# Optimization experiments

Hardware: AMD Instinct MI355X
Metric: run time of the kernel (lower is better)

The kernel has to match this reference:

```python
import jax, jax.numpy as jnp
import numpy as np

GROUP_SIZE = 128
IN_FEATURES = 4096
OUT_FEATURES = 4096
BATCH, SEQ = 4, 2048


def setup_inputs() -> dict:
    key = jax.random.key(0)
    k1, k2, k3, k4 = jax.random.split(key, 4)
    x = jax.random.normal(k1, (BATCH, SEQ, IN_FEATURES), dtype=jnp.float32)
    # packed int4 pairs: values in [0, 256), semantics of uint8
    weight_packed = jax.random.randint(k2, (OUT_FEATURES, IN_FEATURES // 2), 0, 256, dtype=jnp.int32)
    groups = IN_FEATURES // GROUP_SIZE  # 32
    scales = jax.random.uniform(k3, (OUT_FEATURES, groups), dtype=jnp.float32) * 0.02 + 0.001
    zeros = jnp.zeros((OUT_FEATURES, groups), dtype=jnp.float32)  # unused in forward (as in source)
    bias = jax.random.normal(k4, (OUT_FEATURES,), dtype=jnp.float32)
    return {"x": x, "weight_packed": weight_packed, "scales": scales, "zeros": zeros, "bias": bias}


def _unpack_int4(packed, K):
    # low nibble -> even columns, high nibble -> odd columns; values shifted to [-8, 7]
    low = (packed & 15) - 8
    high = ((packed >> 4) & 15) - 8
    M = packed.shape[0]
    return jnp.stack([low, high], axis=-1).reshape(M, K)  # interleave [l0,h0,l1,h1,...]


def reference(x, weight_packed, scales, zeros, bias):
    K = IN_FEATURES
    groups = K // GROUP_SIZE
    w_int = _unpack_int4(weight_packed, K)  # [O, K] int
    w_grouped = w_int.astype(jnp.float32).reshape(OUT_FEATURES, groups, GROUP_SIZE)
    w = (w_grouped * scales[:, :, None]).reshape(OUT_FEATURES, K).astype(x.dtype)
    # F.linear: x @ w^T + bias
    return jnp.einsum('bsk,ok->bso', x, w) + bias
```

## Files before the change

kernel.cpp:

```cpp
#include <hip/hip_runtime.h>


typedef int i32x4 __attribute__((ext_vector_type(4)));

#define GAS __attribute__((address_space(1)))
#define LAS __attribute__((address_space(3)))

static constexpr int M_DIM = 8192;
static constexpr int N_DIM = 4096;
static constexpr int K_DIM = 4096;

__global__ __launch_bounds__(256) void quant_x(const float* __restrict__ x,
                                               signed char* __restrict__ xq,
                                               float* __restrict__ sx) {
    const int row = blockIdx.x;
    const int tid = threadIdx.x;
    const float* xr = x + (size_t)row * K_DIM;
    float4 v[4];
#pragma unroll
    for (int i = 0; i < 4; ++i) v[i] = *(const float4*)(xr + i * 1024 + tid * 4);
    float m = 0.f;
#pragma unroll
    for (int i = 0; i < 4; ++i)
        m = fmaxf(m, fmaxf(fmaxf(fabsf(v[i].x), fabsf(v[i].y)),
                           fmaxf(fabsf(v[i].z), fabsf(v[i].w))));
#pragma unroll
    for (int off = 32; off >= 1; off >>= 1) m = fmaxf(m, __shfl_xor(m, off, 64));
    __shared__ float wm[4];
    if ((tid & 63) == 0) wm[tid >> 6] = m;
    __syncthreads();
    m = fmaxf(fmaxf(wm[0], wm[1]), fmaxf(wm[2], wm[3]));
    const float inv = 127.f / m;
    if (tid == 0) sx[row] = m / 127.f;
#pragma unroll
    for (int i = 0; i < 4; ++i) {
        int b0 = (int)rintf(v[i].x * inv) & 255;
        int b1 = (int)rintf(v[i].y * inv) & 255;
        int b2 = (int)rintf(v[i].z * inv) & 255;
        int b3 = (int)rintf(v[i].w * inv) & 255;
        *(int*)(xq + (size_t)row * K_DIM + i * 1024 + tid * 4) =
            b0 | (b1 << 8) | (b2 << 16) | (b3 << 24);
    }
}

__global__ __launch_bounds__(256) void unpack_w(const int* __restrict__ wp,
                                                signed char* __restrict__ wq) {
    const int t = blockIdx.x * 256 + threadIdx.x;
    int4 p = *(const int4*)(wp + (size_t)t * 4);
    int pv[4] = {p.x, p.y, p.z, p.w};
    int w01 = (((pv[0] & 15) - 8) & 255) | (((((pv[0] >> 4) & 15) - 8) & 255) << 8) |
              ((((pv[1] & 15) - 8) & 255) << 16) | (((((pv[1] >> 4) & 15) - 8) & 255) << 24);
    int w23 = (((pv[2] & 15) - 8) & 255) | (((((pv[2] >> 4) & 15) - 8) & 255) << 8) |
              ((((pv[3] & 15) - 8) & 255) << 16) | (((((pv[3] >> 4) & 15) - 8) & 255) << 24);
    *(int2*)(wq + (size_t)t * 8) = make_int2(w01, w23);
}

__global__ __launch_bounds__(256) void transp_scales(const float* __restrict__ s,
                                                     float* __restrict__ st) {
    const int t = blockIdx.x * 256 + threadIdx.x;
    st[(size_t)(t & 31) * N_DIM + (t >> 5)] = s[t];
}


#define STAGE_AH(BUF, H, TAU) do { \
  _Pragma("unroll") \
  for (int r_ = 0; r_ < 2; ++r_) { \
    const int g_ = r_ * 8 + wv; \
    const int rbase_ = (g_ >> 2) * 64 + (H) * 32 + (g_ & 3) * 8; \
    const int c_ = (l & 7) ^ (l >> 3); \
    const signed char* sA_ = Aq + (size_t)(m0 + rbase_ + (l >> 3)) * K_DIM \
                                + (size_t)(TAU) * 128 + c_ * 16; \
    __builtin_amdgcn_global_load_lds((const GAS void*)sA_, \
        (LAS void*)(lds + (BUF) * 32768 + rbase_ * 128), 16, 0, 0); \
  } \
} while (0)

#define STAGE_BH(BUF, H, TAU) do { \
    const int rbase_ = (wv >> 2) * 64 + (H) * 32 + (wv & 3) * 8; \
    const int c_ = (l & 7) ^ (l >> 3); \
    const signed char* sB_ = Bq + (size_t)(n0 + rbase_ + (l >> 3)) * K_DIM \
                                + (size_t)(TAU) * 128 + c_ * 16; \
    __builtin_amdgcn_global_load_lds((const GAS void*)sB_, \
        (LAS void*)(lds + 65536 + (BUF) * 16384 + rbase_ * 128), 16, 0, 0); \
} while (0)

#define LOAD_SJ(DST, G) do { \
  _Pragma("unroll") \
  for (int j_ = 0; j_ < 4; ++j_) \
    DST[j_] = scalesT[(size_t)(G) * N_DIM + n0 + wc * 64 + j_ * 16 + lr]; \
} while (0)

#define PHASE(B, MH, NH, S0, S1) do { \
  i32x4 aF0_[2], aF1_[2], bF0_[2], bF1_[2]; \
  _Pragma("unroll") \
  for (int nj = 0; nj < 2; ++nj) { \
    const int rb = wc * 64 + (NH) * 32 + nj * 16 + lr; \
    const signed char* bp = lds + 65536 + (B) * 16384 + rb * 128; \
    bF0_[nj] = *(const i32x4*)(bp + ((quad       ^ (rb & 7)) << 4)); \
    bF1_[nj] = *(const i32x4*)(bp + (((4 | quad) ^ (rb & 7)) << 4)); \
  } \
  _Pragma("unroll") \
  for (int mi = 0; mi < 2; ++mi) { \
    const int ra = wr * 64 + (MH) * 32 + mi * 16 + lr; \
    const signed char* ap = lds + (B) * 32768 + ra * 128; \
    aF0_[mi] = *(const i32x4*)(ap + ((quad       ^ (ra & 7)) << 4)); \
    aF1_[mi] = *(const i32x4*)(ap + (((4 | quad) ^ (ra & 7)) << 4)); \
  } \
  i32x4 ci_[2][2]; \
  __builtin_amdgcn_s_setprio(1); \
  _Pragma("unroll") \
  for (int mi = 0; mi < 2; ++mi) { \
    ci_[mi][0] = __builtin_amdgcn_mfma_i32_16x16x64_i8(aF0_[mi], bF0_[0], izero, 0, 0, 0); \
    ci_[mi][1] = __builtin_amdgcn_mfma_i32_16x16x64_i8(aF0_[mi], bF0_[1], izero, 0, 0, 0); \
  } \
  _Pragma("unroll") \
  for (int mi = 0; mi < 2; ++mi) { \
    ci_[mi][0] = __builtin_amdgcn_mfma_i32_16x16x64_i8(aF1_[mi], bF1_[0], ci_[mi][0], 0, 0, 0); \
    ci_[mi][1] = __builtin_amdgcn_mfma_i32_16x16x64_i8(aF1_[mi], bF1_[1], ci_[mi][1], 0, 0, 0); \
  } \
  __builtin_amdgcn_s_setprio(0); \
  _Pragma("unroll") \
  for (int mi = 0; mi < 2; ++mi) \
    _Pragma("unroll") \
    for (int r = 0; r < 4; ++r) { \
      accf[(MH) * 2 + mi][(NH) * 2 + 0][r] += (S0) * (float)ci_[mi][0][r]; \
      accf[(MH) * 2 + mi][(NH) * 2 + 1][r] += (S1) * (float)ci_[mi][1][r]; \
    } \
} while (0)

#define VMW(N) asm volatile("s_waitcnt vmcnt(" #N ")" ::: "memory")
#define CLB()  asm volatile("" ::: "memory")
#define BAR()  __builtin_amdgcn_s_barrier()

__global__ __launch_bounds__(512)
__attribute__((amdgpu_waves_per_eu(2, 2)))
void gemm_i8(const signed char* __restrict__ Aq,
             const signed char* __restrict__ Bq,
             const float* __restrict__ scalesT,
             const float* __restrict__ sx,
             const float* __restrict__ bias,
             float* __restrict__ C) {
    __shared__ signed char lds[98304];

    const int tid  = threadIdx.x;
    const int l    = tid & 63;
    const int wv   = tid >> 6;
    const int wr   = wv >> 1;
    const int wc   = wv & 1;
    const int lr   = l & 15;
    const int quad = l >> 4;

    const int bid = blockIdx.x;
    const int xcd = bid & 7, kk = bid >> 3;
    const int by = (xcd >> 1) * 8 + (kk & 7);
    const int bx = (xcd & 1) * 16 + (kk >> 3);
    const int m0 = by * 256, n0 = bx * 128;

    float accf[4][4][4];
#pragma unroll
    for (int i = 0; i < 4; ++i)
#pragma unroll
        for (int j = 0; j < 4; ++j)
#pragma unroll
            for (int r = 0; r < 4; ++r) accf[i][j][r] = 0.f;

    const i32x4 izero = {0, 0, 0, 0};
    float sjc0[4], sjc1[4], sjn0[4], sjn1[4];

    LOAD_SJ(sjc0, 0);
    LOAD_SJ(sjc1, 1);
    STAGE_AH(0, 0, 0);
    STAGE_BH(0, 0, 0);
    STAGE_BH(0, 1, 0);
    STAGE_AH(0, 1, 0);
    VMW(3);
    BAR();

#pragma unroll 1
    for (int it = 0; it < 16; ++it) {
        const int tb  = it * 2 + 1;
        const int tn0 = (it * 2 + 2) & 31;
        const int tn1 = (it * 2 + 3) & 31;

        STAGE_AH(1, 0, tb); LOAD_SJ(sjn0, tn0);
        PHASE(0, 0, 0, sjc0[0], sjc0[1]);
        VMW(8); BAR();

        STAGE_BH(1, 0, tb);
        PHASE(0, 0, 1, sjc0[2], sjc0[3]);
        VMW(7); BAR();

        STAGE_BH(1, 1, tb);
        PHASE(0, 1, 0, sjc0[0], sjc0[1]);
        CLB(); BAR();

        STAGE_AH(1, 1, tb);
        PHASE(0, 1, 1, sjc0[2], sjc0[3]);
        VMW(3); BAR();

        STAGE_AH(0, 0, tn0); LOAD_SJ(sjn1, tn1);
        PHASE(1, 0, 0, sjc1[0], sjc1[1]);
        VMW(8); BAR();

        STAGE_BH(0, 0, tn0);
        PHASE(1, 0, 1, sjc1[2], sjc1[3]);
        VMW(7); BAR();

        STAGE_BH(0, 1, tn0);
        PHASE(1, 1, 0, sjc1[0], sjc1[1]);
        CLB(); BAR();

        STAGE_AH(0, 1, tn0);
        PHASE(1, 1, 1, sjc1[2], sjc1[3]);
        VMW(3); BAR();

#pragma unroll
        for (int j = 0; j < 4; ++j) { sjc0[j] = sjn0[j]; sjc1[j] = sjn1[j]; }
    }

    asm volatile("s_waitcnt vmcnt(0)" ::: "memory");

    float sxr[4][4];
#pragma unroll
    for (int i = 0; i < 4; ++i)
#pragma unroll
        for (int r = 0; r < 4; ++r)
            sxr[i][r] = sx[m0 + wr * 64 + i * 16 + quad * 4 + r];
#pragma unroll
    for (int j = 0; j < 4; ++j) {
        const int gn = n0 + wc * 64 + j * 16 + lr;
        const float bv = bias[gn];
#pragma unroll
        for (int i = 0; i < 4; ++i) {
            const size_t gm = (size_t)m0 + wr * 64 + i * 16 + quad * 4;
#pragma unroll
            for (int r = 0; r < 4; ++r)
                C[(gm + r) * N_DIM + gn] = accf[i][j][r] * sxr[i][r] + bv;
        }
    }
}

extern "C" void kernel_launch(void* const* d_in, const int* in_sizes, int n_in,
                              void* d_out, int out_size, void* d_ws, size_t ws_size,
                              hipStream_t stream) {
    const float* x      = (const float*)d_in[0];
    const int*   wp     = (const int*)d_in[1];
    const float* scales = (const float*)d_in[2];
    const float* bias   = (const float*)d_in[4];
    float* out = (float*)d_out;

    signed char* Xq = (signed char*)d_ws;
    signed char* Wq = (signed char*)d_ws + (size_t)M_DIM * K_DIM;
    float* sx  = (float*)((char*)d_ws + (size_t)M_DIM * K_DIM + (size_t)N_DIM * K_DIM);
    float* scT = (float*)((char*)d_ws + (size_t)M_DIM * K_DIM + (size_t)N_DIM * K_DIM + 32768);

    quant_x<<<M_DIM, 256, 0, stream>>>(x, Xq, sx);
    unpack_w<<<(N_DIM * (K_DIM / 2) / 4) / 256, 256, 0, stream>>>(wp, Wq);
    transp_scales<<<(N_DIM * 32) / 256, 256, 0, stream>>>(scales, scT);
    gemm_i8<<<dim3(1024), 512, 0, stream>>>(Xq, Wq, scT, sx, bias, out);
}
```

Measured before the change: 450.2 us.

## Restructure int8 GEMM main loop into two K-half phases per tile with full 4x4 MFMA

Replaces the four quarter-tile phases per K-tile with two K-half phases, each loading full 4x4 A/B fragments and issuing 16 MFMAs into an int32 accumulator. The float scaling and accumulation now happens once per K-tile (DRAIN) instead of after every phase. Global-to-LDS staging is regrouped into whole-A and whole-B chunks with matching waitcnt values, which halves the barriers per tile. In exchange it needs more registers for the 16 int32 accumulators and the larger fragment sets, and it has coarser load/compute interleaving.

```diff
diff --git a/kernel.cpp b/kernel.cpp
--- a/kernel.cpp
+++ b/kernel.cpp
@@ -62,11 +62,10 @@
 }
 
 
-#define STAGE_AH(BUF, H, TAU) do { \
-  _Pragma("unroll") \
-  for (int r_ = 0; r_ < 2; ++r_) { \
-    const int g_ = r_ * 8 + wv; \
-    const int rbase_ = (g_ >> 2) * 64 + (H) * 32 + (g_ & 3) * 8; \
+#define STAGE_A(BUF, TAU) do { \
+  _Pragma("unroll") \
+  for (int r_ = 0; r_ < 4; ++r_) { \
+    const int rbase_ = (r_ * 8 + wv) * 8; \
     const int c_ = (l & 7) ^ (l >> 3); \
     const signed char* sA_ = Aq + (size_t)(m0 + rbase_ + (l >> 3)) * K_DIM \
                                 + (size_t)(TAU) * 128 + c_ * 16; \
@@ -75,13 +74,16 @@
   } \
 } while (0)
 
-#define STAGE_BH(BUF, H, TAU) do { \
-    const int rbase_ = (wv >> 2) * 64 + (H) * 32 + (wv & 3) * 8; \
+#define STAGE_B(BUF, TAU) do { \
+  _Pragma("unroll") \
+  for (int r_ = 0; r_ < 2; ++r_) { \
+    const int rbase_ = (r_ * 8 + wv) * 8; \
     const int c_ = (l & 7) ^ (l >> 3); \
     const signed char* sB_ = Bq + (size_t)(n0 + rbase_ + (l >> 3)) * K_DIM \
                                 + (size_t)(TAU) * 128 + c_ * 16; \
     __builtin_amdgcn_global_load_lds((const GAS void*)sB_, \
         (LAS void*)(lds + 65536 + (BUF) * 16384 + rbase_ * 128), 16, 0, 0); \
+  } \
 } while (0)
 
 #define LOAD_SJ(DST, G) do { \
@@ -90,47 +92,43 @@
     DST[j_] = scalesT[(size_t)(G) * N_DIM + n0 + wc * 64 + j_ * 16 + lr]; \
 } while (0)
 
-#define PHASE(B, MH, NH, S0, S1) do { \
-  i32x4 aF0_[2], aF1_[2], bF0_[2], bF1_[2]; \
-  _Pragma("unroll") \
-  for (int nj = 0; nj < 2; ++nj) { \
-    const int rb = wc * 64 + (NH) * 32 + nj * 16 + lr; \
-    const signed char* bp = lds + 65536 + (B) * 16384 + rb * 128; \
-    bF0_[nj] = *(const i32x4*)(bp + ((quad       ^ (rb & 7)) << 4)); \
-    bF1_[nj] = *(const i32x4*)(bp + (((4 | quad) ^ (rb & 7)) << 4)); \
-  } \
-  _Pragma("unroll") \
-  for (int mi = 0; mi < 2; ++mi) { \
-    const int ra = wr * 64 + (MH) * 32 + mi * 16 + lr; \
-    const signed char* ap = lds + (B) * 32768 + ra * 128; \
-    aF0_[mi] = *(const i32x4*)(ap + ((quad       ^ (ra & 7)) << 4)); \
-    aF1_[mi] = *(const i32x4*)(ap + (((4 | quad) ^ (ra & 7)) << 4)); \
-  } \
-  i32x4 ci_[2][2]; \
+#define PHASE_MFMA(B, KS, INIT) do { \
+  i32x4 aF_[4], bF_[4]; \
+  _Pragma("unroll") \
+  for (int nj = 0; nj < 4; ++nj) { \
+    const int rb = wc * 64 + nj * 16 + lr; \
+    bF_[nj] = *(const i32x4*)(lds + 65536 + (B) * 16384 + rb * 128 \
+                              + ((((KS) * 4 + quad) ^ (rb & 7)) << 4)); \
+  } \
+  _Pragma("unroll") \
+  for (int mi = 0; mi < 4; ++mi) { \
+    const int ra = wr * 64 + mi * 16 + lr; \
+    aF_[mi] = *(const i32x4*)(lds + (B) * 32768 + ra * 128 \
+                              + ((((KS) * 4 + quad) ^ (ra & 7)) << 4)); \
+  } \
   __builtin_amdgcn_s_setprio(1); \
   _Pragma("unroll") \
-  for (int mi = 0; mi < 2; ++mi) { \
-    ci_[mi][0] = __builtin_amdgcn_mfma_i32_16x16x64_i8(aF0_[mi], bF0_[0], izero, 0, 0, 0); \
-    ci_[mi][1] = __builtin_amdgcn_mfma_i32_16x16x64_i8(aF0_[mi], bF0_[1], izero, 0, 0, 0); \
-  } \
-  _Pragma("unroll") \
-  for (int mi = 0; mi < 2; ++mi) { \
-    ci_[mi][0] = __builtin_amdgcn_mfma_i32_16x16x64_i8(aF1_[mi], bF1_[0], ci_[mi][0], 0, 0, 0); \
-    ci_[mi][1] = __builtin_amdgcn_mfma_i32_16x16x64_i8(aF1_[mi], bF1_[1], ci_[mi][1], 0, 0, 0); \
-  } \
+  for (int mi = 0; mi < 4; ++mi) \
+    _Pragma("unroll") \
+    for (int nj = 0; nj < 4; ++nj) \
+      ci[mi][nj] = __builtin_amdgcn_mfma_i32_16x16x64_i8( \
+          aF_[mi], bF_[nj], (INIT) ? izero : ci[mi][nj], 0, 0, 0); \
   __builtin_amdgcn_s_setprio(0); \
-  _Pragma("unroll") \
-  for (int mi = 0; mi < 2; ++mi) \
+} while (0)
+
+#define DRAIN(SJ) do { \
+  _Pragma("unroll") \
+  for (int mi = 0; mi < 4; ++mi) \
     _Pragma("unroll") \
-    for (int r = 0; r < 4; ++r) { \
-      accf[(MH) * 2 + mi][(NH) * 2 + 0][r] += (S0) * (float)ci_[mi][0][r]; \
-      accf[(MH) * 2 + mi][(NH) * 2 + 1][r] += (S1) * (float)ci_[mi][1][r]; \
-    } \
+    for (int nj = 0; nj < 4; ++nj) \
+      _Pragma("unroll") \
+      for (int r = 0; r < 4; ++r) \
+        accf[mi][nj][r] += (SJ)[nj] * (float)ci[mi][nj][r]; \
 } while (0)
 
 #define VMW(N) asm volatile("s_waitcnt vmcnt(" #N ")" ::: "memory")
 #define CLB()  asm volatile("" ::: "memory")
-#define BAR()  __builtin_amdgcn_s_barrier()
+#define BAR()  do { __builtin_amdgcn_s_barrier(); asm volatile("" ::: "memory"); } while (0)
 
 __global__ __launch_bounds__(512)
 __attribute__((amdgpu_waves_per_eu(2, 2)))
@@ -167,52 +165,40 @@
     const i32x4 izero = {0, 0, 0, 0};
     float sjc0[4], sjc1[4], sjn0[4], sjn1[4];
 
+    STAGE_A(0, 0);
+    STAGE_B(0, 0);
     LOAD_SJ(sjc0, 0);
     LOAD_SJ(sjc1, 1);
-    STAGE_AH(0, 0, 0);
-    STAGE_BH(0, 0, 0);
-    STAGE_BH(0, 1, 0);
-    STAGE_AH(0, 1, 0);
-    VMW(3);
+    VMW(8);
     BAR();
 
 #pragma unroll 1
     for (int it = 0; it < 16; ++it) {
-        const int tb  = it * 2 + 1;
+        const int t1  = it * 2 + 1;
         const int tn0 = (it * 2 + 2) & 31;
         const int tn1 = (it * 2 + 3) & 31;
 
-        STAGE_AH(1, 0, tb); LOAD_SJ(sjn0, tn0);
-        PHASE(0, 0, 0, sjc0[0], sjc0[1]);
+        i32x4 ci[4][4];
+
+        STAGE_A(1, t1);
+        PHASE_MFMA(0, 0, 1);
         VMW(8); BAR();
 
-        STAGE_BH(1, 0, tb);
-        PHASE(0, 0, 1, sjc0[2], sjc0[3]);
-        VMW(7); BAR();
-
-        STAGE_BH(1, 1, tb);
-        PHASE(0, 1, 0, sjc0[0], sjc0[1]);
+        STAGE_B(1, t1);
+        LOAD_SJ(sjn0, tn0);
+        PHASE_MFMA(0, 1, 0);
+        DRAIN(sjc0);
+        VMW(4); BAR();
+
+        STAGE_A(0, tn0);
+        PHASE_MFMA(1, 0, 1);
         CLB(); BAR();
 
-        STAGE_AH(1, 1, tb);
-        PHASE(0, 1, 1, sjc0[2], sjc0[3]);
-        VMW(3); BAR();
-
-        STAGE_AH(0, 0, tn0); LOAD_SJ(sjn1, tn1);
-        PHASE(1, 0, 0, sjc1[0], sjc1[1]);
-        VMW(8); BAR();
-
-        STAGE_BH(0, 0, tn0);
-        PHASE(1, 0, 1, sjc1[2], sjc1[3]);
-        VMW(7); BAR();
-
-        STAGE_BH(0, 1, tn0);
-        PHASE(1, 1, 0, sjc1[0], sjc1[1]);
-        CLB(); BAR();
-
-        STAGE_AH(0, 1, tn0);
-        PHASE(1, 1, 1, sjc1[2], sjc1[3]);
-        VMW(3); BAR();
+        STAGE_B(0, tn0);
+        LOAD_SJ(sjn1, tn1);
+        PHASE_MFMA(1, 1, 0);
+        DRAIN(sjc1);
+        VMW(4); BAR();
 
 #pragma unroll
         for (int j = 0; j < 4; ++j) { sjc0[j] = sjn0[j]; sjc1[j] = sjn1[j]; }
```

After: 706.1 us. 1.57x slower.
